# Kernel tuning notes

Measured on AMD Instinct MI355X. Metric: run time of the kernel, lower is better.

## Reference

```python
import jax, jax.numpy as jnp
import numpy as np

N, L, C, S = 4096, 512, 16, 32


def setup_inputs() -> dict:
    key = jax.random.key(0)
    k1, k2, k3, k4 = jax.random.split(key, 4)
    raw = jax.random.normal(k1, (N, L, C), dtype=jnp.float32)
    # valid log-probs: logsumexp along C is slightly < 0
    log_input_probs = jax.nn.log_softmax(raw, axis=-1) - 0.01
    return {
        "log_input_probs": log_input_probs,
        "logit_initial_state_probs": jax.random.normal(k2, (S,), dtype=jnp.float32),
        "logit_transition_probs": jax.random.normal(k3, (S, C, S), dtype=jnp.float32),
        "logit_accepting_state_probs": jax.random.normal(k4, (S,), dtype=jnp.float32),
    }


def reference(log_input_probs, logit_initial_state_probs, logit_transition_probs,
              logit_accepting_state_probs):
    initial_state_probs = jax.nn.softmax(logit_initial_state_probs, axis=0)          # (S,)
    transition_probs = jax.nn.softmax(logit_transition_probs, axis=2)                # (S,C,S)
    accepting_log = jax.nn.log_sigmoid(logit_accepting_state_probs)                  # (S,)
    input_probs = jnp.exp(log_input_probs)                                           # (N,L,C)

    n = log_input_probs.shape[0]
    p0 = jnp.broadcast_to(initial_state_probs[None, :], (n, initial_state_probs.shape[0]))

    def step(p_state, x_t):
        # p_state: (N,S) prev-state probs; x_t: (N,C) symbol probs at step t
        p_new = jnp.einsum('bp,bc,pcn->bn', p_state, x_t, transition_probs)
        return p_new, None

    xs = jnp.swapaxes(input_probs, 0, 1)  # (L,N,C) for scan over time
    p_final, _ = jax.lax.scan(step, p0, xs)

    log_p_state = jnp.log(p_final + 1e-20)                                           # (N,S)
    log_acceptance = jax.nn.logsumexp(log_p_state + accepting_log[None, :], axis=1)  # (N,)
    return log_acceptance[None]  # (1,N)
```

## Files before the change

kernel.cpp:

```cpp
#include <hip/hip_runtime.h>
#include <math.h>

typedef _Float16 f16;
typedef _Float16 f16x2 __attribute__((ext_vector_type(2)));
typedef _Float16 f16x4 __attribute__((ext_vector_type(4)));
typedef _Float16 f16x8 __attribute__((ext_vector_type(8)));
typedef float    f32x4 __attribute__((ext_vector_type(4)));

#define NB 4096
#define LT 512
#define NC 16
#define NS 32

#define WS_P0     0
#define WS_SIG    128
#define WS_SUMSIG 256
#define WS_FWDT   512
#define WS_BWDT   (512 + 32768)
#define WS_F      (512 + 65536)
#define WS_G      (WS_F + 32*4096*4)

#if __has_builtin(__builtin_amdgcn_exp2f)
#define EXP2F __builtin_amdgcn_exp2f
#else
#define EXP2F exp2f
#endif

__global__ __launch_bounds__(512) void pdfa_prep(const float* __restrict__ tlogit,
                                                 const float* __restrict__ ilogit,
                                                 const float* __restrict__ alogit,
                                                 char* __restrict__ ws) {
    int tid = threadIdx.x;
    f16* fwdT = (f16*)(ws + WS_FWDT);
    f16* bwdT = (f16*)(ws + WS_BWDT);
    int p = tid >> 4, c = tid & 15;
    const float* row = tlogit + p * 512 + c * 32;
    float mx = row[0];
    for (int n = 1; n < 32; ++n) mx = fmaxf(mx, row[n]);
    float s = 0.f;
    for (int n = 0; n < 32; ++n) s += expf(row[n] - mx);
    float inv = 1.f / s;
    int chalf = c >> 3, j = c & 7;
    for (int n = 0; n < 32; ++n) {
        float tv = expf(row[n] - mx) * inv;
        fwdT[((((p >> 2) * 2 + ((p >> 1) & 1)) * 2 + (n >> 4)) * 64
              + 16 * (2 * (p & 1) + chalf) + (n & 15)) * 8 + j] = (f16)tv;
        bwdT[((((n >> 2) * 2 + ((n >> 1) & 1)) * 2 + (p >> 4)) * 64
              + 16 * (2 * (n & 1) + chalf) + (p & 15)) * 8 + j] = (f16)tv;
    }
    if (tid < 32) {
        float m0 = ilogit[0];
        for (int n = 1; n < 32; ++n) m0 = fmaxf(m0, ilogit[n]);
        float s0 = 0.f;
        for (int n = 0; n < 32; ++n) s0 += expf(ilogit[n] - m0);
        ((float*)(ws + WS_P0))[tid]  = 256.f * expf(ilogit[tid] - m0) / s0;
        ((float*)(ws + WS_SIG))[tid] = 256.f / (1.f + expf(-alogit[tid]));
    }
    if (tid == 0) {
        float ss = 0.f;
        for (int n = 0; n < 32; ++n) ss += 1.f / (1.f + expf(-alogit[n]));
        *(float*)(ws + WS_SUMSIG) = ss;
    }
}

#define EC(v) ((f16)EXP2F((v) * 1.44269504089f))

#define XBUF_OFF 16384

#define STEP(P, XRAW, TNEXT) { \
    f16 p0_ = h32 ? pnew[1] : pnew[0]; \
    f16 p1_ = h32 ? pnew[3] : pnew[2]; \
    f16x8 pb0_ = {p0_, p0_, p0_, p0_, p0_, p0_, p0_, p0_}; \
    f16x8 pb1_ = {p1_, p1_, p1_, p1_, p1_, p1_, p1_, p1_}; \
    f16x8 b0_ = pb0_ * xq8; \
    f16x8 b1_ = pb1_ * xq8; \
    __builtin_amdgcn_s_setprio(1); \
    f32x4 aR0_ = __builtin_amdgcn_mfma_f32_16x16x32_f16(af[0][0], b0_, z4, 0, 0, 0); \
    f32x4 aR1_ = __builtin_amdgcn_mfma_f32_16x16x32_f16(af[1][0], b0_, z4, 0, 0, 0); \
    aR0_ = __builtin_amdgcn_mfma_f32_16x16x32_f16(af[0][1], b1_, aR0_, 0, 0, 0); \
    aR1_ = __builtin_amdgcn_mfma_f32_16x16x32_f16(af[1][1], b1_, aR1_, 0, 0, 0); \
    __builtin_amdgcn_s_setprio(0); \
    char* wp_ = lds + (P) * 8192 + w * 1024 + lane * 8; \
    *(f16x4*)(wp_)       = f16x4{(f16)aR0_[0], (f16)aR0_[1], (f16)aR0_[2], (f16)aR0_[3]}; \
    *(f16x4*)(wp_ + 512) = f16x4{(f16)aR1_[0], (f16)aR1_[1], (f16)aR1_[2], (f16)aR1_[3]}; \
    if (produce) { \
        *(f16*)(xw + (((P)^1)) * 768) = EC(XRAW); \
        XRAW = xg[(size_t)(TNEXT) * NC]; \
    } \
    __syncthreads(); \
    const char* rp_ = lds + (P) * 8192 + (w >> 2) * 512 + (w & 3) * 128 + col * 8; \
    f16x4 q0_ = *(const f16x4*)(rp_); \
    f16x4 q1_ = *(const f16x4*)(rp_ + 1024); \
    f16x4 q2_ = *(const f16x4*)(rp_ + 2048); \
    f16x4 q3_ = *(const f16x4*)(rp_ + 3072); \
    f16x4 q4_ = *(const f16x4*)(rp_ + 4096); \
    f16x4 q5_ = *(const f16x4*)(rp_ + 5120); \
    f16x4 q6_ = *(const f16x4*)(rp_ + 6144); \
    f16x4 q7_ = *(const f16x4*)(rp_ + 7168); \
    xq8 = *(const f16x8*)(xr_base + (((P)^1)) * 768); \
    pnew = ((q0_ + q1_) + (q2_ + q3_)) + ((q4_ + q5_) + (q6_ + q7_)); }

__global__ __launch_bounds__(512, 4) void pdfa_main(const float* __restrict__ login,
                                                    char* __restrict__ ws) {
    __shared__ __align__(16) char lds[2 * 8192 + 2 * 768];
    const int tid  = threadIdx.x;
    const int w    = tid >> 6;
    const int lane = tid & 63;
    const int col  = lane & 15;
    const int chalf = (lane >> 4) & 1;
    const int h32  = lane >> 5;
    const int bid  = blockIdx.x;
    const int dir  = bid & 1;
    const int b0   = (bid >> 1) << 4;

    const char* tblb = ws + (dir ? WS_BWDT : WS_FWDT);
    f16x8 af[2][2];
#pragma unroll
    for (int r = 0; r < 2; ++r)
#pragma unroll
        for (int kc = 0; kc < 2; ++kc)
            af[r][kc] = *(const f16x8*)(tblb + (((w * 2 + kc) * 2 + r) * 64 + lane) * 16);

    const float* initv = (const float*)(ws + (dir ? WS_SIG : WS_P0));
    f16x4 pnew;
#pragma unroll
    for (int j = 0; j < 4; ++j) pnew[j] = (f16)initv[4 * w + j];

    const bool produce = (tid < 256);
    const int colv = (tid >> 4) & 15, cv = tid & 15;
    const float* xg = login + (size_t)(b0 + colv) * (LT * NC) + cv;
    char* xw = lds + XBUF_OFF + colv * 48 + (cv >> 3) * 16 + (cv & 7) * 2;
    const char* xr_base = lds + XBUF_OFF + col * 48 + chalf * 16;

    const f32x4 z4{};
    f16x8 xq8;
    float xrA = 0.f, xrB = 0.f;

#define TT(S) (dir ? (511 - (S)) : (S))
    if (produce) {
        xrA = xg[(size_t)TT(0) * NC];
        xrB = xg[(size_t)TT(1) * NC];
        *(f16*)(xw) = EC(xrA);
        xrA = xg[(size_t)TT(2) * NC];
    }
    __syncthreads();
    xq8 = *(const f16x8*)(xr_base);

    for (int s = 0; s < 256; s += 2) {
        STEP(0, xrB, TT(s + 3))
        STEP(1, xrA, TT(s + 4))
    }
#undef TT

    if (lane < 16) {
        float* outv = (float*)(ws + (dir ? WS_G : WS_F));
#pragma unroll
        for (int j = 0; j < 4; ++j)
            outv[(size_t)(4 * w + j) * NB + b0 + col] = (float)pnew[j];
    }
}

__global__ __launch_bounds__(256) void pdfa_combine(const char* __restrict__ ws,
                                                    float* __restrict__ out) {
    int b = blockIdx.x * 256 + threadIdx.x;
    const float* f = (const float*)(ws + WS_F);
    const float* g = (const float*)(ws + WS_G);
    float ss = *(const float*)(ws + WS_SUMSIG);
    float dot = 0.f;
#pragma unroll
    for (int s2 = 0; s2 < 32; ++s2)
        dot = fmaf(f[s2 * NB + b], g[s2 * NB + b], dot);
    out[b] = logf(dot * (1.f / 65536.f) + 1e-20f * ss);
}

extern "C" void kernel_launch(void* const* d_in, const int* in_sizes, int n_in,
                              void* d_out, int out_size, void* d_ws, size_t ws_size,
                              hipStream_t stream) {
    const float* login = (const float*)d_in[0];
    const float* ilog  = (const float*)d_in[1];
    const float* tlog  = (const float*)d_in[2];
    const float* alog  = (const float*)d_in[3];
    char* ws = (char*)d_ws;

    pdfa_prep<<<1, 512, 0, stream>>>(tlog, ilog, alog, ws);
    pdfa_main<<<512, 512, 0, stream>>>(login, ws);
    pdfa_combine<<<NB / 256, 256, 0, stream>>>(ws, (float*)d_out);
}
```

Baseline: 143.4 us.

## Halve waves per block, give each wave eight states and four k-chunks

Each block of the sequential scan now runs 4 waves instead of 8. Each wave owns 8 previous-state rows, issues 8 MFMAs in two independent accumulation chains, and sums them in registers before writing to LDS. This halves the cross-wave LDS reduction (4 wide reads instead of 8 narrow ones) and the number of waves meeting at each per-step barrier. The LDS layouts get padding to limit bank conflicts. The cost is more serial MFMA work per wave on the critical path and fewer waves available to hide latency.

Result: slower. 325.1 us (+126.7%).

```diff
diff --git a/kernel.cpp b/kernel.cpp
--- a/kernel.cpp
+++ b/kernel.cpp
@@ -43,9 +43,9 @@
     int chalf = c >> 3, j = c & 7;
     for (int n = 0; n < 32; ++n) {
         float tv = expf(row[n] - mx) * inv;
-        fwdT[((((p >> 2) * 2 + ((p >> 1) & 1)) * 2 + (n >> 4)) * 64
+        fwdT[((((p >> 3) * 4 + ((p >> 1) & 3)) * 2 + (n >> 4)) * 64
               + 16 * (2 * (p & 1) + chalf) + (n & 15)) * 8 + j] = (f16)tv;
-        bwdT[((((n >> 2) * 2 + ((n >> 1) & 1)) * 2 + (p >> 4)) * 64
+        bwdT[((((n >> 3) * 4 + ((n >> 1) & 3)) * 2 + (p >> 4)) * 64
               + 16 * (2 * (n & 1) + chalf) + (p & 15)) * 8 + j] = (f16)tv;
     }
     if (tid < 32) {
@@ -65,86 +65,84 @@
 
 #define EC(v) ((f16)EXP2F((v) * 1.44269504089f))
 
-#define XBUF_OFF 16384
+#define PBUF 4608
+#define XOFF 9216
+#define XB   640
 
 #define STEP(P, XRAW, TNEXT) { \
-    f16 p0_ = h32 ? pnew[1] : pnew[0]; \
-    f16 p1_ = h32 ? pnew[3] : pnew[2]; \
-    f16x8 pb0_ = {p0_, p0_, p0_, p0_, p0_, p0_, p0_, p0_}; \
-    f16x8 pb1_ = {p1_, p1_, p1_, p1_, p1_, p1_, p1_, p1_}; \
-    f16x8 b0_ = pb0_ * xq8; \
-    f16x8 b1_ = pb1_ * xq8; \
+    f16x8 bf0_, bf1_, bf2_, bf3_; \
+    { f16 pv_ = h32 ? pnew[1] : pnew[0]; f16x8 pb_ = {pv_,pv_,pv_,pv_,pv_,pv_,pv_,pv_}; bf0_ = pb_ * xq8; } \
+    { f16 pv_ = h32 ? pnew[3] : pnew[2]; f16x8 pb_ = {pv_,pv_,pv_,pv_,pv_,pv_,pv_,pv_}; bf1_ = pb_ * xq8; } \
+    { f16 pv_ = h32 ? pnew[5] : pnew[4]; f16x8 pb_ = {pv_,pv_,pv_,pv_,pv_,pv_,pv_,pv_}; bf2_ = pb_ * xq8; } \
+    { f16 pv_ = h32 ? pnew[7] : pnew[6]; f16x8 pb_ = {pv_,pv_,pv_,pv_,pv_,pv_,pv_,pv_}; bf3_ = pb_ * xq8; } \
     __builtin_amdgcn_s_setprio(1); \
-    f32x4 aR0_ = __builtin_amdgcn_mfma_f32_16x16x32_f16(af[0][0], b0_, z4, 0, 0, 0); \
-    f32x4 aR1_ = __builtin_amdgcn_mfma_f32_16x16x32_f16(af[1][0], b0_, z4, 0, 0, 0); \
-    aR0_ = __builtin_amdgcn_mfma_f32_16x16x32_f16(af[0][1], b1_, aR0_, 0, 0, 0); \
-    aR1_ = __builtin_amdgcn_mfma_f32_16x16x32_f16(af[1][1], b1_, aR1_, 0, 0, 0); \
+    f32x4 c0_ = __builtin_amdgcn_mfma_f32_16x16x32_f16(af[0][0], bf0_, z4, 0, 0, 0); \
+    f32x4 c1_ = __builtin_amdgcn_mfma_f32_16x16x32_f16(af[1][0], bf0_, z4, 0, 0, 0); \
+    f32x4 c2_ = __builtin_amdgcn_mfma_f32_16x16x32_f16(af[0][1], bf1_, z4, 0, 0, 0); \
+    f32x4 c3_ = __builtin_amdgcn_mfma_f32_16x16x32_f16(af[1][1], bf1_, z4, 0, 0, 0); \
+    c0_ = __builtin_amdgcn_mfma_f32_16x16x32_f16(af[0][2], bf2_, c0_, 0, 0, 0); \
+    c1_ = __builtin_amdgcn_mfma_f32_16x16x32_f16(af[1][2], bf2_, c1_, 0, 0, 0); \
+    c2_ = __builtin_amdgcn_mfma_f32_16x16x32_f16(af[0][3], bf3_, c2_, 0, 0, 0); \
+    c3_ = __builtin_amdgcn_mfma_f32_16x16x32_f16(af[1][3], bf3_, c3_, 0, 0, 0); \
     __builtin_amdgcn_s_setprio(0); \
-    char* wp_ = lds + (P) * 8192 + w * 1024 + lane * 8; \
-    *(f16x4*)(wp_)       = f16x4{(f16)aR0_[0], (f16)aR0_[1], (f16)aR0_[2], (f16)aR0_[3]}; \
-    *(f16x4*)(wp_ + 512) = f16x4{(f16)aR1_[0], (f16)aR1_[1], (f16)aR1_[2], (f16)aR1_[3]}; \
-    if (produce) { \
-        *(f16*)(xw + (((P)^1)) * 768) = EC(XRAW); \
-        XRAW = xg[(size_t)(TNEXT) * NC]; \
-    } \
+    f32x4 r0_ = c0_ + c2_, r1_ = c1_ + c3_; \
+    char* wp_ = lds + (P) * PBUF + w * 1152 + col * 72 + 8 * h4; \
+    *(f16x4*)(wp_)      = f16x4{(f16)r0_[0], (f16)r0_[1], (f16)r0_[2], (f16)r0_[3]}; \
+    *(f16x4*)(wp_ + 32) = f16x4{(f16)r1_[0], (f16)r1_[1], (f16)r1_[2], (f16)r1_[3]}; \
+    *(f16*)(xw + (((P)^1)) * XB) = EC(XRAW); \
+    XRAW = xg[(size_t)(TNEXT) * NC]; \
     __syncthreads(); \
-    const char* rp_ = lds + (P) * 8192 + (w >> 2) * 512 + (w & 3) * 128 + col * 8; \
-    f16x4 q0_ = *(const f16x4*)(rp_); \
-    f16x4 q1_ = *(const f16x4*)(rp_ + 1024); \
-    f16x4 q2_ = *(const f16x4*)(rp_ + 2048); \
-    f16x4 q3_ = *(const f16x4*)(rp_ + 3072); \
-    f16x4 q4_ = *(const f16x4*)(rp_ + 4096); \
-    f16x4 q5_ = *(const f16x4*)(rp_ + 5120); \
-    f16x4 q6_ = *(const f16x4*)(rp_ + 6144); \
-    f16x4 q7_ = *(const f16x4*)(rp_ + 7168); \
-    xq8 = *(const f16x8*)(xr_base + (((P)^1)) * 768); \
-    pnew = ((q0_ + q1_) + (q2_ + q3_)) + ((q4_ + q5_) + (q6_ + q7_)); }
+    const char* rp_ = lds + (P) * PBUF + col * 72 + 16 * w; \
+    f16x8 q0_ = *(const f16x8*)(rp_); \
+    f16x8 q1_ = *(const f16x8*)(rp_ + 1152); \
+    f16x8 q2_ = *(const f16x8*)(rp_ + 2304); \
+    f16x8 q3_ = *(const f16x8*)(rp_ + 3456); \
+    xq8 = *(const f16x8*)(xr + (((P)^1)) * XB); \
+    pnew = (q0_ + q1_) + (q2_ + q3_); }
 
-__global__ __launch_bounds__(512, 4) void pdfa_main(const float* __restrict__ login,
+__global__ __launch_bounds__(256, 2) void pdfa_main(const float* __restrict__ login,
                                                     char* __restrict__ ws) {
-    __shared__ __align__(16) char lds[2 * 8192 + 2 * 768];
+    __shared__ __align__(16) char lds[2 * PBUF + 2 * XB];
     const int tid  = threadIdx.x;
     const int w    = tid >> 6;
     const int lane = tid & 63;
     const int col  = lane & 15;
-    const int chalf = (lane >> 4) & 1;
+    const int h4   = lane >> 4;
+    const int chalf = h4 & 1;
     const int h32  = lane >> 5;
     const int bid  = blockIdx.x;
     const int dir  = bid & 1;
     const int b0   = (bid >> 1) << 4;
 
     const char* tblb = ws + (dir ? WS_BWDT : WS_FWDT);
-    f16x8 af[2][2];
+    f16x8 af[2][4];
 #pragma unroll
     for (int r = 0; r < 2; ++r)
 #pragma unroll
-        for (int kc = 0; kc < 2; ++kc)
-            af[r][kc] = *(const f16x8*)(tblb + (((w * 2 + kc) * 2 + r) * 64 + lane) * 16);
+        for (int kc = 0; kc < 4; ++kc)
+            af[r][kc] = *(const f16x8*)(tblb + (((w * 4 + kc) * 2 + r) * 64 + lane) * 16);
 
     const float* initv = (const float*)(ws + (dir ? WS_SIG : WS_P0));
-    f16x4 pnew;
+    f16x8 pnew;
 #pragma unroll
-    for (int j = 0; j < 4; ++j) pnew[j] = (f16)initv[4 * w + j];
+    for (int j = 0; j < 8; ++j) pnew[j] = (f16)initv[8 * w + j];
 
-    const bool produce = (tid < 256);
     const int colv = (tid >> 4) & 15, cv = tid & 15;
     const float* xg = login + (size_t)(b0 + colv) * (LT * NC) + cv;
-    char* xw = lds + XBUF_OFF + colv * 48 + (cv >> 3) * 16 + (cv & 7) * 2;
-    const char* xr_base = lds + XBUF_OFF + col * 48 + chalf * 16;
+    char* xw = lds + XOFF + colv * 40 + cv * 2;
+    const char* xr = lds + XOFF + col * 40 + chalf * 16;
 
     const f32x4 z4{};
     f16x8 xq8;
-    float xrA = 0.f, xrB = 0.f;
+    float xrA, xrB;
 
 #define TT(S) (dir ? (511 - (S)) : (S))
-    if (produce) {
-        xrA = xg[(size_t)TT(0) * NC];
-        xrB = xg[(size_t)TT(1) * NC];
-        *(f16*)(xw) = EC(xrA);
-        xrA = xg[(size_t)TT(2) * NC];
-    }
+    xrA = xg[(size_t)TT(0) * NC];
+    xrB = xg[(size_t)TT(1) * NC];
+    *(f16*)(xw) = EC(xrA);
+    xrA = xg[(size_t)TT(2) * NC];
     __syncthreads();
-    xq8 = *(const f16x8*)(xr_base);
+    xq8 = *(const f16x8*)(xr);
 
     for (int s = 0; s < 256; s += 2) {
         STEP(0, xrB, TT(s + 3))
@@ -152,11 +150,11 @@
     }
 #undef TT
 
-    if (lane < 16) {
+    if (h4 == 0) {
         float* outv = (float*)(ws + (dir ? WS_G : WS_F));
 #pragma unroll
-        for (int j = 0; j < 4; ++j)
-            outv[(size_t)(4 * w + j) * NB + b0 + col] = (float)pnew[j];
+        for (int j = 0; j < 8; ++j)
+            outv[(size_t)(8 * w + j) * NB + b0 + col] = (float)pnew[j];
     }
 }
 
@@ -183,6 +181,6 @@
     char* ws = (char*)d_ws;
 
     pdfa_prep<<<1, 512, 0, stream>>>(tlog, ilog, alog, ws);
-    pdfa_main<<<512, 512, 0, stream>>>(login, ws);
+    pdfa_main<<<512, 256, 0, stream>>>(login, ws);
     pdfa_combine<<<NB / 256, 256, 0, stream>>>(ws, (float*)d_out);
 }
```
